# Kernel tuning notes

Measured on AMD Instinct MI355X. Metric: run time of the kernel, lower is better.

## Reference

```python
import jax, jax.numpy as jnp
import numpy as np

NEG_SLOPE = 0.2


def gat_conv(x, src, dst, W, a_src, a_dst, b, heads, ch, n_nodes):
    # x: [N, F_in] -> h: [N, H, C]
    h = (x @ W).reshape(n_nodes, heads, ch)
    alpha_src = (h * a_src).sum(-1)  # [N, H]
    alpha_dst = (h * a_dst).sum(-1)  # [N, H]
    e = jax.nn.leaky_relu(alpha_src[src] + alpha_dst[dst], NEG_SLOPE)  # [E, H]
    # segment softmax over destination neighborhoods (every node has a self-loop)
    m = jax.ops.segment_max(e, dst, num_segments=n_nodes)
    e = jnp.exp(e - m[dst])
    s = jax.ops.segment_sum(e, dst, num_segments=n_nodes)
    alpha = e / s[dst]  # [E, H]
    out = jax.ops.segment_sum(h[src] * alpha[:, :, None], dst, num_segments=n_nodes)
    return out.reshape(n_nodes, heads * ch) + b


def setup_inputs() -> dict:
    key = jax.random.key(0)
    ks = jax.random.split(key, 12)
    N, E = 50000, 800000
    F_in, HID, H, OUT = 128, 64, 2, 64
    x = jax.random.normal(ks[0], (N, F_in), dtype=jnp.float32)
    edge_index = jax.random.randint(ks[1], (2, E), 0, N, dtype=jnp.int64)
    s1 = 1.0 / np.sqrt(F_in)
    s2 = 1.0 / np.sqrt(H * HID)
    return {
        "x": x,
        "edge_index": edge_index,
        "W1": jax.random.normal(ks[2], (F_in, H * HID), dtype=jnp.float32) * s1,
        "att_src1": jax.random.normal(ks[3], (H, HID), dtype=jnp.float32) * s1,
        "att_dst1": jax.random.normal(ks[4], (H, HID), dtype=jnp.float32) * s1,
        "b1": jnp.zeros((H * HID,), dtype=jnp.float32),
        "W2": jax.random.normal(ks[5], (H * HID, OUT), dtype=jnp.float32) * s2,
        "att_src2": jax.random.normal(ks[6], (1, OUT), dtype=jnp.float32) * s2,
        "att_dst2": jax.random.normal(ks[7], (1, OUT), dtype=jnp.float32) * s2,
        "b2": jnp.zeros((OUT,), dtype=jnp.float32),
    }


def reference(x, edge_index, W1, att_src1, att_dst1, b1, W2, att_src2, att_dst2, b2):
    N = x.shape[0]
    # PyG GATConv adds self-loops by default
    loops = jnp.arange(N, dtype=edge_index.dtype)
    src = jnp.concatenate([edge_index[0], loops])
    dst = jnp.concatenate([edge_index[1], loops])
    h = gat_conv(x, src, dst, W1, att_src1, att_dst1, b1, 2, 64, N)
    h = jax.nn.relu(h)
    out = gat_conv(h, src, dst, W2, att_src2, att_dst2, b2, 1, 64, N)
    return jax.nn.sigmoid(out)
```

## Files before the change

### kernel.cpp

```cpp
#include <hip/hip_runtime.h>
#include <math.h>

#define N_NODES 50000
#define N_EDGES 800000
#define NEG_SLOPE 0.2f
#define NB_BKT  ((N_NODES + 127) / 128)
#define BKT_CAP 3200
#define P1_CHUNK 4096
#define NB_P1   ((N_EDGES + P1_CHUNK - 1) / P1_CHUNK)
#define NB_G1   ((N_NODES + 127) / 128)
#define CELL_CAP 48

typedef short bf16x8 __attribute__((ext_vector_type(8)));
typedef float f32x4 __attribute__((ext_vector_type(4)));

static __device__ __forceinline__ float lrelu(float v) {
    return v > 0.0f ? v : NEG_SLOPE * v;
}

static __device__ __forceinline__ unsigned short f2bf(float f) {
    unsigned b = __float_as_uint(f);
    return (unsigned short)((b + 0x7fffu + ((b >> 16) & 1u)) >> 16);
}

static __device__ __forceinline__ float bflo(unsigned u) { return __uint_as_float(u << 16); }
static __device__ __forceinline__ float bfhi(unsigned u) { return __uint_as_float(u & 0xffff0000u); }

static __device__ __forceinline__ int swz(int row, int k) {
    return row * 128 + ((((k >> 3) ^ (row & 15)) << 3) | (k & 7));
}
static __device__ __forceinline__ int swz64(int row, int c) {
    return row * 64 + ((((c >> 3) ^ (row & 7)) << 3) | (c & 7));
}

__global__ __launch_bounds__(256) void scatterP1_kernel(const int* __restrict__ ei,
                                                        int* __restrict__ cellcnt,
                                                        unsigned* __restrict__ cells) {
    __shared__ int cnt[NB_BKT];
    int tid = threadIdx.x;
    int c = blockIdx.x;
    for (int i = tid; i < NB_BKT; i += 256) cnt[i] = 0;
    __syncthreads();
    int cbase = c * P1_CHUNK;
    for (int i = tid; i < P1_CHUNK; i += 256) {
        int e = cbase + i;
        if (e >= N_EDGES) break;
        int s = ei[e];
        int d = ei[N_EDGES + e];
        int bk = d >> 7;
        int pos = atomicAdd(&cnt[bk], 1);
        if (pos < CELL_CAP)
            cells[(size_t)(c * NB_BKT + bk) * CELL_CAP + pos] =
                ((unsigned)s << 7) | (unsigned)(d & 127);
    }
    __syncthreads();
    for (int i = tid; i < NB_BKT; i += 256) {
        int v = cnt[i];
        cellcnt[c * NB_BKT + i] = v < CELL_CAP ? v : CELL_CAP;
    }
}

__global__ __launch_bounds__(256, 4) void fusedB_kernel(const float* __restrict__ x,
                                                        const float* __restrict__ W,
                                                        const float* __restrict__ a_src,
                                                        const float* __restrict__ a_dst,
                                                        unsigned short* __restrict__ h1b,
                                                        float* __restrict__ as_out,
                                                        float* __restrict__ ad_out,
                                                        const int* __restrict__ cellcnt,
                                                        const unsigned* __restrict__ cells,
                                                        int* __restrict__ offsets,
                                                        int* __restrict__ deg,
                                                        int* __restrict__ csr_src) {
    __shared__ __align__(16) unsigned char smem[32768];
    int tid = threadIdx.x;

    if (blockIdx.x < NB_BKT) {
        int* cnt   = (int*)smem;
        int* scn   = (int*)(smem + 1024);
        int* sst   = (int*)(smem + 2048);
        int* cincl = (int*)(smem + 3072);
        int* fkeys = (int*)(smem + 4096);
        int* lsrc  = (int*)(smem + 4096 + 4 * BKT_CAP);
        int t = tid;
        int b = blockIdx.x;
        int pbase = b * BKT_CAP;
        int node0 = b << 7;
        int nloc = N_NODES - node0; if (nloc > 128) nloc = 128;

        cnt[t] = (t < nloc) ? 1 : 0;
        cincl[t] = (t < NB_P1) ? cellcnt[t * NB_BKT + b] : 0;
        __syncthreads();
#pragma unroll
        for (int off = 1; off < 256; off <<= 1) {
            int u = (t >= off) ? cincl[t - off] : 0;
            __syncthreads();
            cincl[t] += u;
            __syncthreads();
        }
        int cntE = cincl[255];
        for (int j = t; j < cntE; j += 256) {
            int lo = 0, hi = NB_P1 - 1;
            while (lo < hi) {
                int mid = (lo + hi) >> 1;
                if (cincl[mid] <= j) lo = mid + 1; else hi = mid;
            }
            int cb2 = lo ? cincl[lo - 1] : 0;
            int k = (int)cells[(size_t)(lo * NB_BKT + b) * CELL_CAP + (j - cb2)];
            fkeys[j] = k;
            atomicAdd(&cnt[k & 127], 1);
        }
        if (t < nloc) fkeys[cntE + t] = ((node0 + t) << 7) | t;
        int cntE2 = cntE + nloc;
        __syncthreads();
        int v = cnt[t];
        scn[t] = v;
        __syncthreads();
#pragma unroll
        for (int off = 1; off < 256; off <<= 1) {
            int u = (t >= off) ? scn[t - off] : 0;
            __syncthreads();
            scn[t] += u;
            __syncthreads();
        }
        int lstart = scn[t] - v;
        sst[t] = lstart;
        cnt[t] = lstart;
        if (t < nloc) {
            offsets[node0 + t] = pbase + lstart;
            deg[node0 + t] = v;
        }
        __syncthreads();
        for (int j = t; j < cntE2; j += 256) {
            int k = fkeys[j];
            int p = atomicAdd(&cnt[k & 127], 1);
            lsrc[p] = k;
        }
        __syncthreads();
        for (int j = t; j < cntE2; j += 256) {
            int w = lsrc[j];
            int dl = w & 127;
            int st = sst[dl];
            int en = scn[dl];
            int r = 0;
            for (int k = st; k < en; ++k) {
                int wk = lsrc[k];
                r += (wk < w) ? 1 : ((wk == w && k < j) ? 1 : 0);
            }
            csr_src[pbase + st + r] = (int)(((unsigned)w) >> 7);
        }
        return;
    }

    unsigned short* wt = (unsigned short*)smem;
    int r0 = (blockIdx.x - NB_BKT) * 128;

    {
        int n = tid & 127;
        int c0 = (tid >> 7) * 8;
        for (int c = c0; c < c0 + 8; ++c) {
            int kb = c * 8;
            ushort4 lo, hi;
            lo.x = f2bf(W[(kb + 0) * 128 + n]);
            lo.y = f2bf(W[(kb + 1) * 128 + n]);
            lo.z = f2bf(W[(kb + 2) * 128 + n]);
            lo.w = f2bf(W[(kb + 3) * 128 + n]);
            hi.x = f2bf(W[(kb + 4) * 128 + n]);
            hi.y = f2bf(W[(kb + 5) * 128 + n]);
            hi.z = f2bf(W[(kb + 6) * 128 + n]);
            hi.w = f2bf(W[(kb + 7) * 128 + n]);
            int a = swz(n, kb);
            *(ushort4*)&wt[a] = lo;
            *(ushort4*)&wt[a + 4] = hi;
        }
    }
    __syncthreads();

    int wv = tid >> 6, lane = tid & 63, lm = lane & 15, quad = lane >> 4;
    int row0 = r0 + wv * 32 + lm;
    int row1 = row0 + 16;
    if (row0 > N_NODES - 1) row0 = N_NODES - 1;
    if (row1 > N_NODES - 1) row1 = N_NODES - 1;

    f32x4 acc[2][8];
#pragma unroll
    for (int m = 0; m < 2; ++m)
#pragma unroll
        for (int n = 0; n < 8; ++n) acc[m][n] = (f32x4){0.f, 0.f, 0.f, 0.f};

#pragma unroll
    for (int kc = 0; kc < 4; ++kc) {
        int kb = kc * 32 + quad * 8;
        float4 va0 = *(const float4*)&x[row0 * 128 + kb];
        float4 va1 = *(const float4*)&x[row0 * 128 + kb + 4];
        float4 vb0 = *(const float4*)&x[row1 * 128 + kb];
        float4 vb1 = *(const float4*)&x[row1 * 128 + kb + 4];
        bf16x8 a0, a1;
        a0[0] = (short)f2bf(va0.x); a0[1] = (short)f2bf(va0.y);
        a0[2] = (short)f2bf(va0.z); a0[3] = (short)f2bf(va0.w);
        a0[4] = (short)f2bf(va1.x); a0[5] = (short)f2bf(va1.y);
        a0[6] = (short)f2bf(va1.z); a0[7] = (short)f2bf(va1.w);
        a1[0] = (short)f2bf(vb0.x); a1[1] = (short)f2bf(vb0.y);
        a1[2] = (short)f2bf(vb0.z); a1[3] = (short)f2bf(vb0.w);
        a1[4] = (short)f2bf(vb1.x); a1[5] = (short)f2bf(vb1.y);
        a1[6] = (short)f2bf(vb1.z); a1[7] = (short)f2bf(vb1.w);
#pragma unroll
        for (int nt = 0; nt < 8; ++nt) {
            bf16x8 bfr = *(bf16x8*)&wt[swz(nt * 16 + lm, kb)];
            acc[0][nt] = __builtin_amdgcn_mfma_f32_16x16x32_bf16(a0, bfr, acc[0][nt], 0, 0, 0);
            acc[1][nt] = __builtin_amdgcn_mfma_f32_16x16x32_bf16(a1, bfr, acc[1][nt], 0, 0, 0);
        }
    }

    float asv[8], adv[8];
#pragma unroll
    for (int nt = 0; nt < 8; ++nt) {
        asv[nt] = a_src[nt * 16 + lm];
        adv[nt] = a_dst[nt * 16 + lm];
    }
#pragma unroll
    for (int mt = 0; mt < 2; ++mt) {
#pragma unroll
        for (int r = 0; r < 4; ++r) {
            float s0 = 0.f, s1 = 0.f, d0 = 0.f, d1 = 0.f;
#pragma unroll
            for (int nt = 0; nt < 4; ++nt) {
                s0 += acc[mt][nt][r] * asv[nt];
                d0 += acc[mt][nt][r] * adv[nt];
            }
#pragma unroll
            for (int nt = 4; nt < 8; ++nt) {
                s1 += acc[mt][nt][r] * asv[nt];
                d1 += acc[mt][nt][r] * adv[nt];
            }
#pragma unroll
            for (int m = 1; m < 16; m <<= 1) {
                s0 += __shfl_xor(s0, m, 64);
                s1 += __shfl_xor(s1, m, 64);
                d0 += __shfl_xor(d0, m, 64);
                d1 += __shfl_xor(d1, m, 64);
            }
            if (lm == 0) {
                int gr = r0 + wv * 32 + mt * 16 + quad * 4 + r;
                if (gr < N_NODES) {
                    as_out[gr * 2 + 0] = s0;
                    as_out[gr * 2 + 1] = s1;
                    ad_out[gr * 2 + 0] = d0;
                    ad_out[gr * 2 + 1] = d1;
                }
            }
        }
    }

    __syncthreads();
#pragma unroll
    for (int mt = 0; mt < 2; ++mt) {
#pragma unroll
        for (int nt = 0; nt < 8; ++nt) {
#pragma unroll
            for (int r = 0; r < 4; ++r) {
                int lrow = wv * 32 + mt * 16 + quad * 4 + r;
                wt[swz(lrow, nt * 16 + lm)] = f2bf(acc[mt][nt][r]);
            }
        }
    }
    __syncthreads();
    {
        int lrow = tid >> 1;
        int cb = (tid & 1) * 64;
        int gr = r0 + lrow;
        if (gr < N_NODES) {
            unsigned short* dst = h1b + (size_t)gr * 128 + cb;
#pragma unroll
            for (int c = 0; c < 8; ++c)
                *(uint4*)(dst + c * 8) = *(uint4*)&wt[swz(lrow, cb + c * 8)];
        }
    }
}

__global__ __launch_bounds__(256, 4) void gemm2_kernel(const unsigned short* __restrict__ xb,
                                                       const float* __restrict__ W,
                                                       const float* __restrict__ a_src,
                                                       const float* __restrict__ a_dst,
                                                       unsigned short* __restrict__ h2b,
                                                       float* __restrict__ as_out,
                                                       float* __restrict__ ad_out) {
    __shared__ unsigned short wt[64 * 128];
    int tid = threadIdx.x;
    int r0 = blockIdx.x * 128;

    {
        int n = tid & 63;
        int c0 = (tid >> 6) * 4;
        for (int c = c0; c < c0 + 4; ++c) {
            int kb = c * 8;
            ushort4 lo, hi;
            lo.x = f2bf(W[(kb + 0) * 64 + n]);
            lo.y = f2bf(W[(kb + 1) * 64 + n]);
            lo.z = f2bf(W[(kb + 2) * 64 + n]);
            lo.w = f2bf(W[(kb + 3) * 64 + n]);
            hi.x = f2bf(W[(kb + 4) * 64 + n]);
            hi.y = f2bf(W[(kb + 5) * 64 + n]);
            hi.z = f2bf(W[(kb + 6) * 64 + n]);
            hi.w = f2bf(W[(kb + 7) * 64 + n]);
            int a = swz(n, kb);
            *(ushort4*)&wt[a] = lo;
            *(ushort4*)&wt[a + 4] = hi;
        }
    }
    __syncthreads();

    int wv = tid >> 6, lane = tid & 63, lm = lane & 15, quad = lane >> 4;
    int row0 = r0 + wv * 32 + lm;
    int row1 = row0 + 16;
    if (row0 > N_NODES - 1) row0 = N_NODES - 1;
    if (row1 > N_NODES - 1) row1 = N_NODES - 1;

    f32x4 acc[2][4];
#pragma unroll
    for (int m = 0; m < 2; ++m)
#pragma unroll
        for (int n = 0; n < 4; ++n) acc[m][n] = (f32x4){0.f, 0.f, 0.f, 0.f};

#pragma unroll
    for (int kc = 0; kc < 4; ++kc) {
        int kb = kc * 32 + quad * 8;
        bf16x8 a0 = *(const bf16x8*)&xb[row0 * 128 + kb];
        bf16x8 a1 = *(const bf16x8*)&xb[row1 * 128 + kb];
#pragma unroll
        for (int nt = 0; nt < 4; ++nt) {
            bf16x8 b = *(bf16x8*)&wt[swz(nt * 16 + lm, kb)];
            acc[0][nt] = __builtin_amdgcn_mfma_f32_16x16x32_bf16(a0, b, acc[0][nt], 0, 0, 0);
            acc[1][nt] = __builtin_amdgcn_mfma_f32_16x16x32_bf16(a1, b, acc[1][nt], 0, 0, 0);
        }
    }

    float asv[4], adv[4];
#pragma unroll
    for (int nt = 0; nt < 4; ++nt) {
        asv[nt] = a_src[nt * 16 + lm];
        adv[nt] = a_dst[nt * 16 + lm];
    }
#pragma unroll
    for (int mt = 0; mt < 2; ++mt) {
#pragma unroll
        for (int r = 0; r < 4; ++r) {
            float s0 = 0.f, d0 = 0.f;
#pragma unroll
            for (int nt = 0; nt < 4; ++nt) {
                s0 += acc[mt][nt][r] * asv[nt];
                d0 += acc[mt][nt][r] * adv[nt];
            }
#pragma unroll
            for (int m = 1; m < 16; m <<= 1) {
                s0 += __shfl_xor(s0, m, 64);
                d0 += __shfl_xor(d0, m, 64);
            }
            if (lm == 0) {
                int gr = r0 + wv * 32 + mt * 16 + quad * 4 + r;
                if (gr < N_NODES) {
                    as_out[gr] = s0;
                    ad_out[gr] = d0;
                }
            }
        }
    }

    __syncthreads();
#pragma unroll
    for (int mt = 0; mt < 2; ++mt) {
#pragma unroll
        for (int nt = 0; nt < 4; ++nt) {
#pragma unroll
            for (int r = 0; r < 4; ++r) {
                int lrow = wv * 32 + mt * 16 + quad * 4 + r;
                wt[swz64(lrow, nt * 16 + lm)] = f2bf(acc[mt][nt][r]);
            }
        }
    }
    __syncthreads();
    {
        int lrow = tid >> 1;
        int cb = (tid & 1) * 32;
        int gr = r0 + lrow;
        if (gr < N_NODES) {
            unsigned short* dst = h2b + (size_t)gr * 64 + cb;
#pragma unroll
            for (int c = 0; c < 4; ++c)
                *(uint4*)(dst + c * 8) = *(uint4*)&wt[swz64(lrow, cb + c * 8)];
        }
    }
}

__global__ void agg1_kernel(const unsigned short* __restrict__ h1b,
                            const float* __restrict__ as1,
                            const float* __restrict__ ad1, const float* __restrict__ b1,
                            const int* __restrict__ offsets, const int* __restrict__ deg,
                            const int* __restrict__ csr_src,
                            unsigned short* __restrict__ out1b) {
    int wid = (blockIdx.x * blockDim.x + threadIdx.x) >> 6;
    if (wid >= N_NODES) return;
    int lane = threadIdx.x & 63;
    int cl = lane & 31;
    int half = lane >> 5;
    bool head1 = (cl >= 16);
    float da0 = ad1[wid * 2 + 0], da1 = ad1[wid * 2 + 1];
    int jb = offsets[wid], je = jb + deg[wid];
    float a0 = 0.f, a1 = 0.f, a2 = 0.f, a3 = 0.f;
    float psum0 = 0.f, psum1 = 0.f;

    for (int chunk = jb; chunk < je; chunk += 64) {
        int j = chunk + lane;
        int s = 0; float w0 = 0.f, w1 = 0.f;
        if (j < je) {
            s = csr_src[j];
            float2 av = *(const float2*)&as1[s * 2];
            w0 = __expf(lrelu(av.x + da0));
            w1 = __expf(lrelu(av.y + da1));
        }
        psum0 += w0; psum1 += w1;
        int cnt = je - chunk; if (cnt > 64) cnt = 64;
        for (int k = 0; k < cnt; k += 8) {
            int k0 = k + half, k1 = k + 2 + half, k2 = k + 4 + half, k3 = k + 6 + half;
            int ss0 = __shfl(s, k0, 64);
            int ss1 = __shfl(s, k1, 64);
            int ss2 = __shfl(s, k2, 64);
            int ss3 = __shfl(s, k3, 64);
            uint2 u0 = ((const uint2*)(h1b + (size_t)ss0 * 128))[cl];
            uint2 u1 = ((const uint2*)(h1b + (size_t)ss1 * 128))[cl];
            uint2 u2 = ((const uint2*)(h1b + (size_t)ss2 * 128))[cl];
            uint2 u3 = ((const uint2*)(h1b + (size_t)ss3 * 128))[cl];
            float p0 = __shfl(w0, k0, 64), q0 = __shfl(w1, k0, 64);
            float p1 = __shfl(w0, k1, 64), q1 = __shfl(w1, k1, 64);
            float p2 = __shfl(w0, k2, 64), q2 = __shfl(w1, k2, 64);
            float p3 = __shfl(w0, k3, 64), q3 = __shfl(w1, k3, 64);
            float bw0 = head1 ? q0 : p0;
            float bw1 = head1 ? q1 : p1;
            float bw2 = head1 ? q2 : p2;
            float bw3 = head1 ? q3 : p3;
            a0 += bw0 * bflo(u0.x); a1 += bw0 * bfhi(u0.x); a2 += bw0 * bflo(u0.y); a3 += bw0 * bfhi(u0.y);
            a0 += bw1 * bflo(u1.x); a1 += bw1 * bfhi(u1.x); a2 += bw1 * bflo(u1.y); a3 += bw1 * bfhi(u1.y);
            a0 += bw2 * bflo(u2.x); a1 += bw2 * bfhi(u2.x); a2 += bw2 * bflo(u2.y); a3 += bw2 * bfhi(u2.y);
            a0 += bw3 * bflo(u3.x); a1 += bw3 * bfhi(u3.x); a2 += bw3 * bflo(u3.y); a3 += bw3 * bfhi(u3.y);
        }
    }
#pragma unroll
    for (int m = 1; m < 64; m <<= 1) {
        psum0 += __shfl_xor(psum0, m, 64);
        psum1 += __shfl_xor(psum1, m, 64);
    }
    float o0 = __shfl(a0, cl + 32, 64);
    float o1 = __shfl(a1, cl + 32, 64);
    float o2 = __shfl(a2, cl + 32, 64);
    float o3 = __shfl(a3, cl + 32, 64);
    if (lane < 32) {
        float inv = 1.f / (head1 ? psum1 : psum0);
        float4 bv = *(const float4*)&b1[cl * 4];
        float v0 = (a0 + o0) * inv + bv.x;
        float v1 = (a1 + o1) * inv + bv.y;
        float v2 = (a2 + o2) * inv + bv.z;
        float v3 = (a3 + o3) * inv + bv.w;
        v0 = v0 > 0.f ? v0 : 0.f;
        v1 = v1 > 0.f ? v1 : 0.f;
        v2 = v2 > 0.f ? v2 : 0.f;
        v3 = v3 > 0.f ? v3 : 0.f;
        ushort4 p;
        p.x = f2bf(v0); p.y = f2bf(v1); p.z = f2bf(v2); p.w = f2bf(v3);
        *(ushort4*)&out1b[(size_t)wid * 128 + cl * 4] = p;
    }
}

__global__ void agg2_kernel(const unsigned short* __restrict__ h2b,
                            const float* __restrict__ as2,
                            const float* __restrict__ ad2, const float* __restrict__ b2,
                            const int* __restrict__ offsets, const int* __restrict__ deg,
                            const int* __restrict__ csr_src,
                            float* __restrict__ out) {
    int wid = (blockIdx.x * blockDim.x + threadIdx.x) >> 6;
    if (wid >= N_NODES) return;
    int lane = threadIdx.x & 63;
    int cl = lane & 31;
    int half = lane >> 5;
    float da = ad2[wid];
    int jb = offsets[wid], je = jb + deg[wid];
    float acc0 = 0.f, acc1 = 0.f, psum = 0.f;

    for (int chunk = jb; chunk < je; chunk += 64) {
        int j = chunk + lane;
        int s = 0; float w = 0.f;
        if (j < je) {
            s = csr_src[j];
            w = __expf(lrelu(as2[s] + da));
        }
        psum += w;
        int cnt = je - chunk; if (cnt > 64) cnt = 64;
        for (int k = 0; k < cnt; k += 8) {
            int k0 = k + half, k1 = k + 2 + half, k2 = k + 4 + half, k3 = k + 6 + half;
            int ss0 = __shfl(s, k0, 64);
            int ss1 = __shfl(s, k1, 64);
            int ss2 = __shfl(s, k2, 64);
            int ss3 = __shfl(s, k3, 64);
            unsigned u0 = ((const unsigned*)(h2b + (size_t)ss0 * 64))[cl];
            unsigned u1 = ((const unsigned*)(h2b + (size_t)ss1 * 64))[cl];
            unsigned u2 = ((const unsigned*)(h2b + (size_t)ss2 * 64))[cl];
            unsigned u3 = ((const unsigned*)(h2b + (size_t)ss3 * 64))[cl];
            float bw0 = __shfl(w, k0, 64);
            float bw1 = __shfl(w, k1, 64);
            float bw2 = __shfl(w, k2, 64);
            float bw3 = __shfl(w, k3, 64);
            acc0 += bw0 * bflo(u0); acc1 += bw0 * bfhi(u0);
            acc0 += bw1 * bflo(u1); acc1 += bw1 * bfhi(u1);
            acc0 += bw2 * bflo(u2); acc1 += bw2 * bfhi(u2);
            acc0 += bw3 * bflo(u3); acc1 += bw3 * bfhi(u3);
        }
    }
#pragma unroll
    for (int m = 1; m < 64; m <<= 1) psum += __shfl_xor(psum, m, 64);
    float o0 = __shfl(acc0, cl + 32, 64);
    float o1 = __shfl(acc1, cl + 32, 64);
    if (lane < 32) {
        float inv = 1.f / psum;
        float2 bv = *(const float2*)&b2[cl * 2];
        float v0 = (acc0 + o0) * inv + bv.x;
        float v1 = (acc1 + o1) * inv + bv.y;
        v0 = 1.f / (1.f + __expf(-v0));
        v1 = 1.f / (1.f + __expf(-v1));
        *(float2*)&out[(size_t)wid * 64 + cl * 2] = make_float2(v0, v1);
    }
}

extern "C" void kernel_launch(void* const* d_in, const int* in_sizes, int n_in,
                              void* d_out, int out_size, void* d_ws, size_t ws_size,
                              hipStream_t stream) {
    const float* x     = (const float*)d_in[0];
    const int*   ei    = (const int*)d_in[1];
    const float* W1    = (const float*)d_in[2];
    const float* asrc1 = (const float*)d_in[3];
    const float* adst1 = (const float*)d_in[4];
    const float* b1    = (const float*)d_in[5];
    const float* W2    = (const float*)d_in[6];
    const float* asrc2 = (const float*)d_in[7];
    const float* adst2 = (const float*)d_in[8];
    const float* b2    = (const float*)d_in[9];
    float* out = (float*)d_out;

    float* ws = (float*)d_ws;
    size_t off = 0;
    float* as1  = ws + off; off += (size_t)N_NODES * 2;
    float* ad1  = ws + off; off += (size_t)N_NODES * 2;
    float* as2  = ws + off; off += (size_t)N_NODES;
    float* ad2  = ws + off; off += (size_t)N_NODES;
    unsigned short* h1b   = (unsigned short*)(ws + off); off += (size_t)N_NODES * 64;
    unsigned short* out1b = (unsigned short*)(ws + off); off += (size_t)N_NODES * 64;
    unsigned short* h2b   = (unsigned short*)(ws + off); off += (size_t)N_NODES * 32;
    int* offsets = (int*)(ws + off);
    int* deg     = offsets + N_NODES;
    int* csr_src = deg + N_NODES;
    int* cellcnt = csr_src + NB_BKT * BKT_CAP;
    unsigned* cells = (unsigned*)(cellcnt + NB_P1 * NB_BKT);

    scatterP1_kernel<<<NB_P1, 256, 0, stream>>>(ei, cellcnt, cells);
    fusedB_kernel<<<NB_BKT + NB_G1, 256, 0, stream>>>(x, W1, asrc1, adst1, h1b, as1, ad1,
                                                      cellcnt, cells, offsets, deg, csr_src);
    agg1_kernel<<<(N_NODES * 64 + 255) / 256, 256, 0, stream>>>(h1b, as1, ad1, b1, offsets, deg, csr_src, out1b);
    gemm2_kernel<<<NB_G1, 256, 0, stream>>>(out1b, W2, asrc2, adst2, h2b, as2, ad2);
    agg2_kernel<<<(N_NODES * 64 + 255) / 256, 256, 0, stream>>>(h2b, as2, ad2, b2, offsets, deg, csr_src, out);
}
```

Before: 193.4 us.

## Process two destination nodes per wavefront in GAT aggregation kernels

Each wavefront in agg1 and agg2 now handles two destination nodes, i and i+N/2, and the grid is halved to match. The first chunk of csr_src indices and attention weights for both nodes is prefetched up front, so those latency-bound loads overlap. Accumulation moves to float2 vector types, which may let the compiler emit packed FMAs, and launch bounds are added. The cost is more registers per lane, the two nodes' gather loops still run one after the other, and half as many waves are available to hide memory latency.

Result: faster. 189.2 us, median of 2 (-2.2%).

```diff
diff --git a/kernel.cpp b/kernel.cpp
--- a/kernel.cpp
+++ b/kernel.cpp
@@ -2,6 +2,7 @@
 #include <math.h>
 
 #define N_NODES 50000
+#define NH (N_NODES / 2)
 #define N_EDGES 800000
 #define NEG_SLOPE 0.2f
 #define NB_BKT  ((N_NODES + 127) / 128)
@@ -13,6 +14,7 @@
 
 typedef short bf16x8 __attribute__((ext_vector_type(8)));
 typedef float f32x4 __attribute__((ext_vector_type(4)));
+typedef float f32x2 __attribute__((ext_vector_type(2)));
 
 static __device__ __forceinline__ float lrelu(float v) {
     return v > 0.0f ? v : NEG_SLOPE * v;
@@ -25,6 +27,9 @@
 
 static __device__ __forceinline__ float bflo(unsigned u) { return __uint_as_float(u << 16); }
 static __device__ __forceinline__ float bfhi(unsigned u) { return __uint_as_float(u & 0xffff0000u); }
+static __device__ __forceinline__ f32x2 bfp(unsigned u) {
+    f32x2 r; r[0] = bflo(u); r[1] = bfhi(u); return r;
+}
 
 static __device__ __forceinline__ int swz(int row, int k) {
     return row * 128 + ((((k >> 3) ^ (row & 15)) << 3) | (k & 7));
@@ -392,34 +397,59 @@
     }
 }
 
-__global__ void agg1_kernel(const unsigned short* __restrict__ h1b,
+__global__ __launch_bounds__(256) void agg1_kernel(const unsigned short* __restrict__ h1b,
                             const float* __restrict__ as1,
                             const float* __restrict__ ad1, const float* __restrict__ b1,
                             const int* __restrict__ offsets, const int* __restrict__ deg,
                             const int* __restrict__ csr_src,
                             unsigned short* __restrict__ out1b) {
-    int wid = (blockIdx.x * blockDim.x + threadIdx.x) >> 6;
-    if (wid >= N_NODES) return;
+    int wv = (blockIdx.x * blockDim.x + threadIdx.x) >> 6;
+    if (wv >= NH) return;
     int lane = threadIdx.x & 63;
     int cl = lane & 31;
     int half = lane >> 5;
     bool head1 = (cl >= 16);
-    float da0 = ad1[wid * 2 + 0], da1 = ad1[wid * 2 + 1];
-    int jb = offsets[wid], je = jb + deg[wid];
-    float a0 = 0.f, a1 = 0.f, a2 = 0.f, a3 = 0.f;
-    float psum0 = 0.f, psum1 = 0.f;
-
-    for (int chunk = jb; chunk < je; chunk += 64) {
-        int j = chunk + lane;
-        int s = 0; float w0 = 0.f, w1 = 0.f;
-        if (j < je) {
-            s = csr_src[j];
-            float2 av = *(const float2*)&as1[s * 2];
-            w0 = __expf(lrelu(av.x + da0));
-            w1 = __expf(lrelu(av.y + da1));
-        }
-        psum0 += w0; psum1 += w1;
-        int cnt = je - chunk; if (cnt > 64) cnt = 64;
+    int widA = wv, widB = wv + NH;
+
+    float2 daA = *(const float2*)&ad1[widA * 2];
+    float2 daB = *(const float2*)&ad1[widB * 2];
+    int jbA = offsets[widA], jeA = jbA + deg[widA];
+    int jbB = offsets[widB], jeB = jbB + deg[widB];
+
+    int jA = jbA + lane, jB = jbB + lane;
+    int spA = 0, spB = 0;
+    float wpA0 = 0.f, wpA1 = 0.f, wpB0 = 0.f, wpB1 = 0.f;
+    if (jA < jeA) spA = csr_src[jA];
+    if (jB < jeB) spB = csr_src[jB];
+    if (jA < jeA) {
+        float2 av = *(const float2*)&as1[spA * 2];
+        wpA0 = __expf(lrelu(av.x + daA.x));
+        wpA1 = __expf(lrelu(av.y + daA.y));
+    }
+    if (jB < jeB) {
+        float2 av = *(const float2*)&as1[spB * 2];
+        wpB0 = __expf(lrelu(av.x + daB.x));
+        wpB1 = __expf(lrelu(av.y + daB.y));
+    }
+
+    f32x2 A0A = (f32x2){0.f, 0.f}, A1A = (f32x2){0.f, 0.f};
+    f32x2 A0B = (f32x2){0.f, 0.f}, A1B = (f32x2){0.f, 0.f};
+    float psA0 = 0.f, psA1 = 0.f, psB0 = 0.f, psB1 = 0.f;
+
+    for (int chunk = jbA; chunk < jeA; chunk += 64) {
+        int s; float w0, w1;
+        if (chunk == jbA) { s = spA; w0 = wpA0; w1 = wpA1; }
+        else {
+            int j = chunk + lane; s = 0; w0 = 0.f; w1 = 0.f;
+            if (j < jeA) {
+                s = csr_src[j];
+                float2 av = *(const float2*)&as1[s * 2];
+                w0 = __expf(lrelu(av.x + daA.x));
+                w1 = __expf(lrelu(av.y + daA.y));
+            }
+        }
+        psA0 += w0; psA1 += w1;
+        int cnt = jeA - chunk; if (cnt > 64) cnt = 64;
         for (int k = 0; k < cnt; k += 8) {
             int k0 = k + half, k1 = k + 2 + half, k2 = k + 4 + half, k3 = k + 6 + half;
             int ss0 = __shfl(s, k0, 64);
@@ -438,62 +468,139 @@
             float bw1 = head1 ? q1 : p1;
             float bw2 = head1 ? q2 : p2;
             float bw3 = head1 ? q3 : p3;
-            a0 += bw0 * bflo(u0.x); a1 += bw0 * bfhi(u0.x); a2 += bw0 * bflo(u0.y); a3 += bw0 * bfhi(u0.y);
-            a0 += bw1 * bflo(u1.x); a1 += bw1 * bfhi(u1.x); a2 += bw1 * bflo(u1.y); a3 += bw1 * bfhi(u1.y);
-            a0 += bw2 * bflo(u2.x); a1 += bw2 * bfhi(u2.x); a2 += bw2 * bflo(u2.y); a3 += bw2 * bfhi(u2.y);
-            a0 += bw3 * bflo(u3.x); a1 += bw3 * bfhi(u3.x); a2 += bw3 * bflo(u3.y); a3 += bw3 * bfhi(u3.y);
-        }
-    }
+            A0A += (f32x2){bw0, bw0} * bfp(u0.x); A1A += (f32x2){bw0, bw0} * bfp(u0.y);
+            A0A += (f32x2){bw1, bw1} * bfp(u1.x); A1A += (f32x2){bw1, bw1} * bfp(u1.y);
+            A0A += (f32x2){bw2, bw2} * bfp(u2.x); A1A += (f32x2){bw2, bw2} * bfp(u2.y);
+            A0A += (f32x2){bw3, bw3} * bfp(u3.x); A1A += (f32x2){bw3, bw3} * bfp(u3.y);
+        }
+    }
+
+    for (int chunk = jbB; chunk < jeB; chunk += 64) {
+        int s; float w0, w1;
+        if (chunk == jbB) { s = spB; w0 = wpB0; w1 = wpB1; }
+        else {
+            int j = chunk + lane; s = 0; w0 = 0.f; w1 = 0.f;
+            if (j < jeB) {
+                s = csr_src[j];
+                float2 av = *(const float2*)&as1[s * 2];
+                w0 = __expf(lrelu(av.x + daB.x));
+                w1 = __expf(lrelu(av.y + daB.y));
+            }
+        }
+        psB0 += w0; psB1 += w1;
+        int cnt = jeB - chunk; if (cnt > 64) cnt = 64;
+        for (int k = 0; k < cnt; k += 8) {
+            int k0 = k + half, k1 = k + 2 + half, k2 = k + 4 + half, k3 = k + 6 + half;
+            int ss0 = __shfl(s, k0, 64);
+            int ss1 = __shfl(s, k1, 64);
+            int ss2 = __shfl(s, k2, 64);
+            int ss3 = __shfl(s, k3, 64);
+            uint2 u0 = ((const uint2*)(h1b + (size_t)ss0 * 128))[cl];
+            uint2 u1 = ((const uint2*)(h1b + (size_t)ss1 * 128))[cl];
+            uint2 u2 = ((const uint2*)(h1b + (size_t)ss2 * 128))[cl];
+            uint2 u3 = ((const uint2*)(h1b + (size_t)ss3 * 128))[cl];
+            float p0 = __shfl(w0, k0, 64), q0 = __shfl(w1, k0, 64);
+            float p1 = __shfl(w0, k1, 64), q1 = __shfl(w1, k1, 64);
+            float p2 = __shfl(w0, k2, 64), q2 = __shfl(w1, k2, 64);
+            float p3 = __shfl(w0, k3, 64), q3 = __shfl(w1, k3, 64);
+            float bw0 = head1 ? q0 : p0;
+            float bw1 = head1 ? q1 : p1;
+            float bw2 = head1 ? q2 : p2;
+            float bw3 = head1 ? q3 : p3;
+            A0B += (f32x2){bw0, bw0} * bfp(u0.x); A1B += (f32x2){bw0, bw0} * bfp(u0.y);
+            A0B += (f32x2){bw1, bw1} * bfp(u1.x); A1B += (f32x2){bw1, bw1} * bfp(u1.y);
+            A0B += (f32x2){bw2, bw2} * bfp(u2.x); A1B += (f32x2){bw2, bw2} * bfp(u2.y);
+            A0B += (f32x2){bw3, bw3} * bfp(u3.x); A1B += (f32x2){bw3, bw3} * bfp(u3.y);
+        }
+    }
+
 #pragma unroll
     for (int m = 1; m < 64; m <<= 1) {
-        psum0 += __shfl_xor(psum0, m, 64);
-        psum1 += __shfl_xor(psum1, m, 64);
-    }
-    float o0 = __shfl(a0, cl + 32, 64);
-    float o1 = __shfl(a1, cl + 32, 64);
-    float o2 = __shfl(a2, cl + 32, 64);
-    float o3 = __shfl(a3, cl + 32, 64);
+        psA0 += __shfl_xor(psA0, m, 64);
+        psA1 += __shfl_xor(psA1, m, 64);
+        psB0 += __shfl_xor(psB0, m, 64);
+        psB1 += __shfl_xor(psB1, m, 64);
+    }
+    float aA0 = A0A[0], aA1 = A0A[1], aA2 = A1A[0], aA3 = A1A[1];
+    float aB0 = A0B[0], aB1 = A0B[1], aB2 = A1B[0], aB3 = A1B[1];
+    float oA0 = __shfl(aA0, cl + 32, 64);
+    float oA1 = __shfl(aA1, cl + 32, 64);
+    float oA2 = __shfl(aA2, cl + 32, 64);
+    float oA3 = __shfl(aA3, cl + 32, 64);
+    float oB0 = __shfl(aB0, cl + 32, 64);
+    float oB1 = __shfl(aB1, cl + 32, 64);
+    float oB2 = __shfl(aB2, cl + 32, 64);
+    float oB3 = __shfl(aB3, cl + 32, 64);
     if (lane < 32) {
-        float inv = 1.f / (head1 ? psum1 : psum0);
         float4 bv = *(const float4*)&b1[cl * 4];
-        float v0 = (a0 + o0) * inv + bv.x;
-        float v1 = (a1 + o1) * inv + bv.y;
-        float v2 = (a2 + o2) * inv + bv.z;
-        float v3 = (a3 + o3) * inv + bv.w;
-        v0 = v0 > 0.f ? v0 : 0.f;
-        v1 = v1 > 0.f ? v1 : 0.f;
-        v2 = v2 > 0.f ? v2 : 0.f;
-        v3 = v3 > 0.f ? v3 : 0.f;
-        ushort4 p;
-        p.x = f2bf(v0); p.y = f2bf(v1); p.z = f2bf(v2); p.w = f2bf(v3);
-        *(ushort4*)&out1b[(size_t)wid * 128 + cl * 4] = p;
-    }
-}
-
-__global__ void agg2_kernel(const unsigned short* __restrict__ h2b,
+        {
+            float inv = 1.f / (head1 ? psA1 : psA0);
+            float v0 = (aA0 + oA0) * inv + bv.x;
+            float v1 = (aA1 + oA1) * inv + bv.y;
+            float v2 = (aA2 + oA2) * inv + bv.z;
+            float v3 = (aA3 + oA3) * inv + bv.w;
+            v0 = v0 > 0.f ? v0 : 0.f;
+            v1 = v1 > 0.f ? v1 : 0.f;
+            v2 = v2 > 0.f ? v2 : 0.f;
+            v3 = v3 > 0.f ? v3 : 0.f;
+            ushort4 p;
+            p.x = f2bf(v0); p.y = f2bf(v1); p.z = f2bf(v2); p.w = f2bf(v3);
+            *(ushort4*)&out1b[(size_t)widA * 128 + cl * 4] = p;
+        }
+        {
+            float inv = 1.f / (head1 ? psB1 : psB0);
+            float v0 = (aB0 + oB0) * inv + bv.x;
+            float v1 = (aB1 + oB1) * inv + bv.y;
+            float v2 = (aB2 + oB2) * inv + bv.z;
+            float v3 = (aB3 + oB3) * inv + bv.w;
+            v0 = v0 > 0.f ? v0 : 0.f;
+            v1 = v1 > 0.f ? v1 : 0.f;
+            v2 = v2 > 0.f ? v2 : 0.f;
+            v3 = v3 > 0.f ? v3 : 0.f;
+            ushort4 p;
+            p.x = f2bf(v0); p.y = f2bf(v1); p.z = f2bf(v2); p.w = f2bf(v3);
+            *(ushort4*)&out1b[(size_t)widB * 128 + cl * 4] = p;
+        }
+    }
+}
+
+__global__ __launch_bounds__(256) void agg2_kernel(const unsigned short* __restrict__ h2b,
                             const float* __restrict__ as2,
                             const float* __restrict__ ad2, const float* __restrict__ b2,
                             const int* __restrict__ offsets, const int* __restrict__ deg,
                             const int* __restrict__ csr_src,
                             float* __restrict__ out) {
-    int wid = (blockIdx.x * blockDim.x + threadIdx.x) >> 6;
-    if (wid >= N_NODES) return;
+    int wv = (blockIdx.x * blockDim.x + threadIdx.x) >> 6;
+    if (wv >= NH) return;
     int lane = threadIdx.x & 63;
     int cl = lane & 31;
     int half = lane >> 5;
-    float da = ad2[wid];
-    int jb = offsets[wid], je = jb + deg[wid];
-    float acc0 = 0.f, acc1 = 0.f, psum = 0.f;
-
-    for (int chunk = jb; chunk < je; chunk += 64) {
-        int j = chunk + lane;
-        int s = 0; float w = 0.f;
-        if (j < je) {
-            s = csr_src[j];
-            w = __expf(lrelu(as2[s] + da));
-        }
-        psum += w;
-        int cnt = je - chunk; if (cnt > 64) cnt = 64;
+    int widA = wv, widB = wv + NH;
+
+    float daA = ad2[widA], daB = ad2[widB];
+    int jbA = offsets[widA], jeA = jbA + deg[widA];
+    int jbB = offsets[widB], jeB = jbB + deg[widB];
+
+    int jA = jbA + lane, jB = jbB + lane;
+    int spA = 0, spB = 0;
+    float wpA = 0.f, wpB = 0.f;
+    if (jA < jeA) spA = csr_src[jA];
+    if (jB < jeB) spB = csr_src[jB];
+    if (jA < jeA) wpA = __expf(lrelu(as2[spA] + daA));
+    if (jB < jeB) wpB = __expf(lrelu(as2[spB] + daB));
+
+    f32x2 AA = (f32x2){0.f, 0.f}, AB = (f32x2){0.f, 0.f};
+    float psA = 0.f, psB = 0.f;
+
+    for (int chunk = jbA; chunk < jeA; chunk += 64) {
+        int s; float w;
+        if (chunk == jbA) { s = spA; w = wpA; }
+        else {
+            int j = chunk + lane; s = 0; w = 0.f;
+            if (j < jeA) { s = csr_src[j]; w = __expf(lrelu(as2[s] + daA)); }
+        }
+        psA += w;
+        int cnt = jeA - chunk; if (cnt > 64) cnt = 64;
         for (int k = 0; k < cnt; k += 8) {
             int k0 = k + half, k1 = k + 2 + half, k2 = k + 4 + half, k3 = k + 6 + half;
             int ss0 = __shfl(s, k0, 64);
@@ -508,24 +615,71 @@
             float bw1 = __shfl(w, k1, 64);
             float bw2 = __shfl(w, k2, 64);
             float bw3 = __shfl(w, k3, 64);
-            acc0 += bw0 * bflo(u0); acc1 += bw0 * bfhi(u0);
-            acc0 += bw1 * bflo(u1); acc1 += bw1 * bfhi(u1);
-            acc0 += bw2 * bflo(u2); acc1 += bw2 * bfhi(u2);
-            acc0 += bw3 * bflo(u3); acc1 += bw3 * bfhi(u3);
-        }
-    }
-#pragma unroll
-    for (int m = 1; m < 64; m <<= 1) psum += __shfl_xor(psum, m, 64);
-    float o0 = __shfl(acc0, cl + 32, 64);
-    float o1 = __shfl(acc1, cl + 32, 64);
+            AA += (f32x2){bw0, bw0} * bfp(u0);
+            AA += (f32x2){bw1, bw1} * bfp(u1);
+            AA += (f32x2){bw2, bw2} * bfp(u2);
+            AA += (f32x2){bw3, bw3} * bfp(u3);
+        }
+    }
+
+    for (int chunk = jbB; chunk < jeB; chunk += 64) {
+        int s; float w;
+        if (chunk == jbB) { s = spB; w = wpB; }
+        else {
+            int j = chunk + lane; s = 0; w = 0.f;
+            if (j < jeB) { s = csr_src[j]; w = __expf(lrelu(as2[s] + daB)); }
+        }
+        psB += w;
+        int cnt = jeB - chunk; if (cnt > 64) cnt = 64;
+        for (int k = 0; k < cnt; k += 8) {
+            int k0 = k + half, k1 = k + 2 + half, k2 = k + 4 + half, k3 = k + 6 + half;
+            int ss0 = __shfl(s, k0, 64);
+            int ss1 = __shfl(s, k1, 64);
+            int ss2 = __shfl(s, k2, 64);
+            int ss3 = __shfl(s, k3, 64);
+            unsigned u0 = ((const unsigned*)(h2b + (size_t)ss0 * 64))[cl];
+            unsigned u1 = ((const unsigned*)(h2b + (size_t)ss1 * 64))[cl];
+            unsigned u2 = ((const unsigned*)(h2b + (size_t)ss2 * 64))[cl];
+            unsigned u3 = ((const unsigned*)(h2b + (size_t)ss3 * 64))[cl];
+            float bw0 = __shfl(w, k0, 64);
+            float bw1 = __shfl(w, k1, 64);
+            float bw2 = __shfl(w, k2, 64);
+            float bw3 = __shfl(w, k3, 64);
+            AB += (f32x2){bw0, bw0} * bfp(u0);
+            AB += (f32x2){bw1, bw1} * bfp(u1);
+            AB += (f32x2){bw2, bw2} * bfp(u2);
+            AB += (f32x2){bw3, bw3} * bfp(u3);
+        }
+    }
+
+#pragma unroll
+    for (int m = 1; m < 64; m <<= 1) {
+        psA += __shfl_xor(psA, m, 64);
+        psB += __shfl_xor(psB, m, 64);
+    }
+    float aA0 = AA[0], aA1 = AA[1], aB0 = AB[0], aB1 = AB[1];
+    float oA0 = __shfl(aA0, cl + 32, 64);
+    float oA1 = __shfl(aA1, cl + 32, 64);
+    float oB0 = __shfl(aB0, cl + 32, 64);
+    float oB1 = __shfl(aB1, cl + 32, 64);
     if (lane < 32) {
-        float inv = 1.f / psum;
         float2 bv = *(const float2*)&b2[cl * 2];
-        float v0 = (acc0 + o0) * inv + bv.x;
-        float v1 = (acc1 + o1) * inv + bv.y;
-        v0 = 1.f / (1.f + __expf(-v0));
-        v1 = 1.f / (1.f + __expf(-v1));
-        *(float2*)&out[(size_t)wid * 64 + cl * 2] = make_float2(v0, v1);
+        {
+            float inv = 1.f / psA;
+            float v0 = (aA0 + oA0) * inv + bv.x;
+            float v1 = (aA1 + oA1) * inv + bv.y;
+            v0 = 1.f / (1.f + __expf(-v0));
+            v1 = 1.f / (1.f + __expf(-v1));
+            *(float2*)&out[(size_t)widA * 64 + cl * 2] = make_float2(v0, v1);
+        }
+        {
+            float inv = 1.f / psB;
+            float v0 = (aB0 + oB0) * inv + bv.x;
+            float v1 = (aB1 + oB1) * inv + bv.y;
+            v0 = 1.f / (1.f + __expf(-v0));
+            v1 = 1.f / (1.f + __expf(-v1));
+            *(float2*)&out[(size_t)widB * 64 + cl * 2] = make_float2(v0, v1);
+        }
     }
 }
 
@@ -562,7 +716,7 @@
     scatterP1_kernel<<<NB_P1, 256, 0, stream>>>(ei, cellcnt, cells);
     fusedB_kernel<<<NB_BKT + NB_G1, 256, 0, stream>>>(x, W1, asrc1, adst1, h1b, as1, ad1,
                                                       cellcnt, cells, offsets, deg, csr_src);
-    agg1_kernel<<<(N_NODES * 64 + 255) / 256, 256, 0, stream>>>(h1b, as1, ad1, b1, offsets, deg, csr_src, out1b);
+    agg1_kernel<<<(NH * 64 + 255) / 256, 256, 0, stream>>>(h1b, as1, ad1, b1, offsets, deg, csr_src, out1b);
     gemm2_kernel<<<NB_G1, 256, 0, stream>>>(out1b, W2, asrc2, adst2, h2b, as2, ad2);
-    agg2_kernel<<<(N_NODES * 64 + 255) / 256, 256, 0, stream>>>(h2b, as2, ad2, b2, offsets, deg, csr_src, out);
-}
+    agg2_kernel<<<(NH * 64 + 255) / 256, 256, 0, stream>>>(h2b, as2, ad2, b2, offsets, deg, csr_src, out);
+}
```

## Process four destination nodes per wavefront in aggregation kernels

Applied to the files above, without the earlier changes.

Each wavefront in agg1 and agg2 now handles four destination nodes, strided by N/4, instead of one. The offsets, degree, first-chunk source indices and attention weights for all four nodes are loaded up front so their memory latencies overlap. Accumulation uses packed float2 vectors, which may let the compiler emit packed FMA instructions. In exchange the grid has four times fewer wavefronts and each thread holds more registers, and the nodes are still processed one after another inside a wave, so latency hiding may depend on occupancy.

Measured after the change: 198.9 us. 1.03x slower.

```diff
diff --git a/kernel.cpp b/kernel.cpp
--- a/kernel.cpp
+++ b/kernel.cpp
@@ -2,6 +2,7 @@
 #include <math.h>
 
 #define N_NODES 50000
+#define NQ (N_NODES / 4)
 #define N_EDGES 800000
 #define NEG_SLOPE 0.2f
 #define NB_BKT  ((N_NODES + 127) / 128)
@@ -13,6 +14,7 @@
 
 typedef short bf16x8 __attribute__((ext_vector_type(8)));
 typedef float f32x4 __attribute__((ext_vector_type(4)));
+typedef float f32x2 __attribute__((ext_vector_type(2)));
 
 static __device__ __forceinline__ float lrelu(float v) {
     return v > 0.0f ? v : NEG_SLOPE * v;
@@ -25,6 +27,9 @@
 
 static __device__ __forceinline__ float bflo(unsigned u) { return __uint_as_float(u << 16); }
 static __device__ __forceinline__ float bfhi(unsigned u) { return __uint_as_float(u & 0xffff0000u); }
+static __device__ __forceinline__ f32x2 bfp(unsigned u) {
+    f32x2 r; r[0] = bflo(u); r[1] = bfhi(u); return r;
+}
 
 static __device__ __forceinline__ int swz(int row, int k) {
     return row * 128 + ((((k >> 3) ^ (row & 15)) << 3) | (k & 7));
@@ -392,140 +397,219 @@
     }
 }
 
-__global__ void agg1_kernel(const unsigned short* __restrict__ h1b,
+__global__ __launch_bounds__(256) void agg1_kernel(const unsigned short* __restrict__ h1b,
                             const float* __restrict__ as1,
                             const float* __restrict__ ad1, const float* __restrict__ b1,
                             const int* __restrict__ offsets, const int* __restrict__ deg,
                             const int* __restrict__ csr_src,
                             unsigned short* __restrict__ out1b) {
-    int wid = (blockIdx.x * blockDim.x + threadIdx.x) >> 6;
-    if (wid >= N_NODES) return;
+    int wv = (blockIdx.x * blockDim.x + threadIdx.x) >> 6;
+    if (wv >= NQ) return;
     int lane = threadIdx.x & 63;
     int cl = lane & 31;
     int half = lane >> 5;
     bool head1 = (cl >= 16);
-    float da0 = ad1[wid * 2 + 0], da1 = ad1[wid * 2 + 1];
-    int jb = offsets[wid], je = jb + deg[wid];
-    float a0 = 0.f, a1 = 0.f, a2 = 0.f, a3 = 0.f;
-    float psum0 = 0.f, psum1 = 0.f;
-
-    for (int chunk = jb; chunk < je; chunk += 64) {
-        int j = chunk + lane;
-        int s = 0; float w0 = 0.f, w1 = 0.f;
-        if (j < je) {
-            s = csr_src[j];
-            float2 av = *(const float2*)&as1[s * 2];
-            w0 = __expf(lrelu(av.x + da0));
-            w1 = __expf(lrelu(av.y + da1));
-        }
-        psum0 += w0; psum1 += w1;
-        int cnt = je - chunk; if (cnt > 64) cnt = 64;
-        for (int k = 0; k < cnt; k += 8) {
-            int k0 = k + half, k1 = k + 2 + half, k2 = k + 4 + half, k3 = k + 6 + half;
-            int ss0 = __shfl(s, k0, 64);
-            int ss1 = __shfl(s, k1, 64);
-            int ss2 = __shfl(s, k2, 64);
-            int ss3 = __shfl(s, k3, 64);
-            uint2 u0 = ((const uint2*)(h1b + (size_t)ss0 * 128))[cl];
-            uint2 u1 = ((const uint2*)(h1b + (size_t)ss1 * 128))[cl];
-            uint2 u2 = ((const uint2*)(h1b + (size_t)ss2 * 128))[cl];
-            uint2 u3 = ((const uint2*)(h1b + (size_t)ss3 * 128))[cl];
-            float p0 = __shfl(w0, k0, 64), q0 = __shfl(w1, k0, 64);
-            float p1 = __shfl(w0, k1, 64), q1 = __shfl(w1, k1, 64);
-            float p2 = __shfl(w0, k2, 64), q2 = __shfl(w1, k2, 64);
-            float p3 = __shfl(w0, k3, 64), q3 = __shfl(w1, k3, 64);
-            float bw0 = head1 ? q0 : p0;
-            float bw1 = head1 ? q1 : p1;
-            float bw2 = head1 ? q2 : p2;
-            float bw3 = head1 ? q3 : p3;
-            a0 += bw0 * bflo(u0.x); a1 += bw0 * bfhi(u0.x); a2 += bw0 * bflo(u0.y); a3 += bw0 * bfhi(u0.y);
-            a0 += bw1 * bflo(u1.x); a1 += bw1 * bfhi(u1.x); a2 += bw1 * bflo(u1.y); a3 += bw1 * bfhi(u1.y);
-            a0 += bw2 * bflo(u2.x); a1 += bw2 * bfhi(u2.x); a2 += bw2 * bflo(u2.y); a3 += bw2 * bfhi(u2.y);
-            a0 += bw3 * bflo(u3.x); a1 += bw3 * bfhi(u3.x); a2 += bw3 * bflo(u3.y); a3 += bw3 * bfhi(u3.y);
-        }
-    }
+
+    int jb[4], je[4], sp[4];
+    float2 da[4];
+    float wp0[4], wp1[4];
+#pragma unroll
+    for (int i = 0; i < 4; ++i) {
+        int wid = wv + i * NQ;
+        da[i] = *(const float2*)&ad1[wid * 2];
+        jb[i] = offsets[wid];
+        je[i] = jb[i] + deg[wid];
+    }
+#pragma unroll
+    for (int i = 0; i < 4; ++i) {
+        int j = jb[i] + lane;
+        sp[i] = (j < je[i]) ? csr_src[j] : 0;
+    }
+#pragma unroll
+    for (int i = 0; i < 4; ++i) {
+        int j = jb[i] + lane;
+        wp0[i] = 0.f; wp1[i] = 0.f;
+        if (j < je[i]) {
+            float2 av = *(const float2*)&as1[sp[i] * 2];
+            wp0[i] = __expf(lrelu(av.x + da[i].x));
+            wp1[i] = __expf(lrelu(av.y + da[i].y));
+        }
+    }
+
+    f32x2 A0[4], A1[4];
+    float ps0[4], ps1[4];
+#pragma unroll
+    for (int i = 0; i < 4; ++i) {
+        A0[i] = (f32x2){0.f, 0.f}; A1[i] = (f32x2){0.f, 0.f};
+        ps0[i] = 0.f; ps1[i] = 0.f;
+    }
+
+#pragma unroll
+    for (int i = 0; i < 4; ++i) {
+        for (int chunk = jb[i]; chunk < je[i]; chunk += 64) {
+            int s; float w0, w1;
+            if (chunk == jb[i]) { s = sp[i]; w0 = wp0[i]; w1 = wp1[i]; }
+            else {
+                int j = chunk + lane; s = 0; w0 = 0.f; w1 = 0.f;
+                if (j < je[i]) {
+                    s = csr_src[j];
+                    float2 av = *(const float2*)&as1[s * 2];
+                    w0 = __expf(lrelu(av.x + da[i].x));
+                    w1 = __expf(lrelu(av.y + da[i].y));
+                }
+            }
+            ps0[i] += w0; ps1[i] += w1;
+            int cnt = je[i] - chunk; if (cnt > 64) cnt = 64;
+            for (int k = 0; k < cnt; k += 8) {
+                int k0 = k + half, k1 = k + 2 + half, k2 = k + 4 + half, k3 = k + 6 + half;
+                int ss0 = __shfl(s, k0, 64);
+                int ss1 = __shfl(s, k1, 64);
+                int ss2 = __shfl(s, k2, 64);
+                int ss3 = __shfl(s, k3, 64);
+                uint2 u0 = ((const uint2*)(h1b + (size_t)ss0 * 128))[cl];
+                uint2 u1 = ((const uint2*)(h1b + (size_t)ss1 * 128))[cl];
+                uint2 u2 = ((const uint2*)(h1b + (size_t)ss2 * 128))[cl];
+                uint2 u3 = ((const uint2*)(h1b + (size_t)ss3 * 128))[cl];
+                float p0 = __shfl(w0, k0, 64), q0 = __shfl(w1, k0, 64);
+                float p1 = __shfl(w0, k1, 64), q1 = __shfl(w1, k1, 64);
+                float p2 = __shfl(w0, k2, 64), q2 = __shfl(w1, k2, 64);
+                float p3 = __shfl(w0, k3, 64), q3 = __shfl(w1, k3, 64);
+                float bw0 = head1 ? q0 : p0;
+                float bw1 = head1 ? q1 : p1;
+                float bw2 = head1 ? q2 : p2;
+                float bw3 = head1 ? q3 : p3;
+                A0[i] += (f32x2){bw0, bw0} * bfp(u0.x); A1[i] += (f32x2){bw0, bw0} * bfp(u0.y);
+                A0[i] += (f32x2){bw1, bw1} * bfp(u1.x); A1[i] += (f32x2){bw1, bw1} * bfp(u1.y);
+                A0[i] += (f32x2){bw2, bw2} * bfp(u2.x); A1[i] += (f32x2){bw2, bw2} * bfp(u2.y);
+                A0[i] += (f32x2){bw3, bw3} * bfp(u3.x); A1[i] += (f32x2){bw3, bw3} * bfp(u3.y);
+            }
+        }
+    }
+
 #pragma unroll
     for (int m = 1; m < 64; m <<= 1) {
-        psum0 += __shfl_xor(psum0, m, 64);
-        psum1 += __shfl_xor(psum1, m, 64);
-    }
-    float o0 = __shfl(a0, cl + 32, 64);
-    float o1 = __shfl(a1, cl + 32, 64);
-    float o2 = __shfl(a2, cl + 32, 64);
-    float o3 = __shfl(a3, cl + 32, 64);
-    if (lane < 32) {
-        float inv = 1.f / (head1 ? psum1 : psum0);
-        float4 bv = *(const float4*)&b1[cl * 4];
-        float v0 = (a0 + o0) * inv + bv.x;
-        float v1 = (a1 + o1) * inv + bv.y;
-        float v2 = (a2 + o2) * inv + bv.z;
-        float v3 = (a3 + o3) * inv + bv.w;
-        v0 = v0 > 0.f ? v0 : 0.f;
-        v1 = v1 > 0.f ? v1 : 0.f;
-        v2 = v2 > 0.f ? v2 : 0.f;
-        v3 = v3 > 0.f ? v3 : 0.f;
-        ushort4 p;
-        p.x = f2bf(v0); p.y = f2bf(v1); p.z = f2bf(v2); p.w = f2bf(v3);
-        *(ushort4*)&out1b[(size_t)wid * 128 + cl * 4] = p;
-    }
-}
-
-__global__ void agg2_kernel(const unsigned short* __restrict__ h2b,
+#pragma unroll
+        for (int i = 0; i < 4; ++i) {
+            ps0[i] += __shfl_xor(ps0[i], m, 64);
+            ps1[i] += __shfl_xor(ps1[i], m, 64);
+        }
+    }
+    float4 bv;
+    if (lane < 32) bv = *(const float4*)&b1[cl * 4];
+#pragma unroll
+    for (int i = 0; i < 4; ++i) {
+        float a0 = A0[i][0], a1 = A0[i][1], a2 = A1[i][0], a3 = A1[i][1];
+        float o0 = __shfl(a0, cl + 32, 64);
+        float o1 = __shfl(a1, cl + 32, 64);
+        float o2 = __shfl(a2, cl + 32, 64);
+        float o3 = __shfl(a3, cl + 32, 64);
+        if (lane < 32) {
+            float inv = 1.f / (head1 ? ps1[i] : ps0[i]);
+            float v0 = (a0 + o0) * inv + bv.x;
+            float v1 = (a1 + o1) * inv + bv.y;
+            float v2 = (a2 + o2) * inv + bv.z;
+            float v3 = (a3 + o3) * inv + bv.w;
+            v0 = v0 > 0.f ? v0 : 0.f;
+            v1 = v1 > 0.f ? v1 : 0.f;
+            v2 = v2 > 0.f ? v2 : 0.f;
+            v3 = v3 > 0.f ? v3 : 0.f;
+            ushort4 p;
+            p.x = f2bf(v0); p.y = f2bf(v1); p.z = f2bf(v2); p.w = f2bf(v3);
+            *(ushort4*)&out1b[(size_t)(wv + i * NQ) * 128 + cl * 4] = p;
+        }
+    }
+}
+
+__global__ __launch_bounds__(256) void agg2_kernel(const unsigned short* __restrict__ h2b,
                             const float* __restrict__ as2,
                             const float* __restrict__ ad2, const float* __restrict__ b2,
                             const int* __restrict__ offsets, const int* __restrict__ deg,
                             const int* __restrict__ csr_src,
                             float* __restrict__ out) {
-    int wid = (blockIdx.x * blockDim.x + threadIdx.x) >> 6;
-    if (wid >= N_NODES) return;
+    int wv = (blockIdx.x * blockDim.x + threadIdx.x) >> 6;
+    if (wv >= NQ) return;
     int lane = threadIdx.x & 63;
     int cl = lane & 31;
     int half = lane >> 5;
-    float da = ad2[wid];
-    int jb = offsets[wid], je = jb + deg[wid];
-    float acc0 = 0.f, acc1 = 0.f, psum = 0.f;
-
-    for (int chunk = jb; chunk < je; chunk += 64) {
-        int j = chunk + lane;
-        int s = 0; float w = 0.f;
-        if (j < je) {
-            s = csr_src[j];
-            w = __expf(lrelu(as2[s] + da));
-        }
-        psum += w;
-        int cnt = je - chunk; if (cnt > 64) cnt = 64;
-        for (int k = 0; k < cnt; k += 8) {
-            int k0 = k + half, k1 = k + 2 + half, k2 = k + 4 + half, k3 = k + 6 + half;
-            int ss0 = __shfl(s, k0, 64);
-            int ss1 = __shfl(s, k1, 64);
-            int ss2 = __shfl(s, k2, 64);
-            int ss3 = __shfl(s, k3, 64);
-            unsigned u0 = ((const unsigned*)(h2b + (size_t)ss0 * 64))[cl];
-            unsigned u1 = ((const unsigned*)(h2b + (size_t)ss1 * 64))[cl];
-            unsigned u2 = ((const unsigned*)(h2b + (size_t)ss2 * 64))[cl];
-            unsigned u3 = ((const unsigned*)(h2b + (size_t)ss3 * 64))[cl];
-            float bw0 = __shfl(w, k0, 64);
-            float bw1 = __shfl(w, k1, 64);
-            float bw2 = __shfl(w, k2, 64);
-            float bw3 = __shfl(w, k3, 64);
-            acc0 += bw0 * bflo(u0); acc1 += bw0 * bfhi(u0);
-            acc0 += bw1 * bflo(u1); acc1 += bw1 * bfhi(u1);
-            acc0 += bw2 * bflo(u2); acc1 += bw2 * bfhi(u2);
-            acc0 += bw3 * bflo(u3); acc1 += bw3 * bfhi(u3);
-        }
-    }
-#pragma unroll
-    for (int m = 1; m < 64; m <<= 1) psum += __shfl_xor(psum, m, 64);
-    float o0 = __shfl(acc0, cl + 32, 64);
-    float o1 = __shfl(acc1, cl + 32, 64);
-    if (lane < 32) {
-        float inv = 1.f / psum;
-        float2 bv = *(const float2*)&b2[cl * 2];
-        float v0 = (acc0 + o0) * inv + bv.x;
-        float v1 = (acc1 + o1) * inv + bv.y;
-        v0 = 1.f / (1.f + __expf(-v0));
-        v1 = 1.f / (1.f + __expf(-v1));
-        *(float2*)&out[(size_t)wid * 64 + cl * 2] = make_float2(v0, v1);
+
+    int jb[4], je[4], sp[4];
+    float da[4], wp[4];
+#pragma unroll
+    for (int i = 0; i < 4; ++i) {
+        int wid = wv + i * NQ;
+        da[i] = ad2[wid];
+        jb[i] = offsets[wid];
+        je[i] = jb[i] + deg[wid];
+    }
+#pragma unroll
+    for (int i = 0; i < 4; ++i) {
+        int j = jb[i] + lane;
+        sp[i] = (j < je[i]) ? csr_src[j] : 0;
+    }
+#pragma unroll
+    for (int i = 0; i < 4; ++i) {
+        int j = jb[i] + lane;
+        wp[i] = (j < je[i]) ? __expf(lrelu(as2[sp[i]] + da[i])) : 0.f;
+    }
+
+    f32x2 A[4];
+    float ps[4];
+#pragma unroll
+    for (int i = 0; i < 4; ++i) { A[i] = (f32x2){0.f, 0.f}; ps[i] = 0.f; }
+
+#pragma unroll
+    for (int i = 0; i < 4; ++i) {
+        for (int chunk = jb[i]; chunk < je[i]; chunk += 64) {
+            int s; float w;
+            if (chunk == jb[i]) { s = sp[i]; w = wp[i]; }
+            else {
+                int j = chunk + lane; s = 0; w = 0.f;
+                if (j < je[i]) { s = csr_src[j]; w = __expf(lrelu(as2[s] + da[i])); }
+            }
+            ps[i] += w;
+            int cnt = je[i] - chunk; if (cnt > 64) cnt = 64;
+            for (int k = 0; k < cnt; k += 8) {
+                int k0 = k + half, k1 = k + 2 + half, k2 = k + 4 + half, k3 = k + 6 + half;
+                int ss0 = __shfl(s, k0, 64);
+                int ss1 = __shfl(s, k1, 64);
+                int ss2 = __shfl(s, k2, 64);
+                int ss3 = __shfl(s, k3, 64);
+                unsigned u0 = ((const unsigned*)(h2b + (size_t)ss0 * 64))[cl];
+                unsigned u1 = ((const unsigned*)(h2b + (size_t)ss1 * 64))[cl];
+                unsigned u2 = ((const unsigned*)(h2b + (size_t)ss2 * 64))[cl];
+                unsigned u3 = ((const unsigned*)(h2b + (size_t)ss3 * 64))[cl];
+                float bw0 = __shfl(w, k0, 64);
+                float bw1 = __shfl(w, k1, 64);
+                float bw2 = __shfl(w, k2, 64);
+                float bw3 = __shfl(w, k3, 64);
+                A[i] += (f32x2){bw0, bw0} * bfp(u0);
+                A[i] += (f32x2){bw1, bw1} * bfp(u1);
+                A[i] += (f32x2){bw2, bw2} * bfp(u2);
+                A[i] += (f32x2){bw3, bw3} * bfp(u3);
+            }
+        }
+    }
+
+#pragma unroll
+    for (int m = 1; m < 64; m <<= 1) {
+#pragma unroll
+        for (int i = 0; i < 4; ++i) ps[i] += __shfl_xor(ps[i], m, 64);
+    }
+    float2 bv;
+    if (lane < 32) bv = *(const float2*)&b2[cl * 2];
+#pragma unroll
+    for (int i = 0; i < 4; ++i) {
+        float a0 = A[i][0], a1 = A[i][1];
+        float o0 = __shfl(a0, cl + 32, 64);
+        float o1 = __shfl(a1, cl + 32, 64);
+        if (lane < 32) {
+            float inv = 1.f / ps[i];
+            float v0 = (a0 + o0) * inv + bv.x;
+            float v1 = (a1 + o1) * inv + bv.y;
+            v0 = 1.f / (1.f + __expf(-v0));
+            v1 = 1.f / (1.f + __expf(-v1));
+            *(float2*)&out[(size_t)(wv + i * NQ) * 64 + cl * 2] = make_float2(v0, v1);
+        }
     }
 }
 
@@ -562,7 +646,7 @@
     scatterP1_kernel<<<NB_P1, 256, 0, stream>>>(ei, cellcnt, cells);
     fusedB_kernel<<<NB_BKT + NB_G1, 256, 0, stream>>>(x, W1, asrc1, adst1, h1b, as1, ad1,
                                                       cellcnt, cells, offsets, deg, csr_src);
-    agg1_kernel<<<(N_NODES * 64 + 255) / 256, 256, 0, stream>>>(h1b, as1, ad1, b1, offsets, deg, csr_src, out1b);
+    agg1_kernel<<<(NQ * 64 + 255) / 256, 256, 0, stream>>>(h1b, as1, ad1, b1, offsets, deg, csr_src, out1b);
     gemm2_kernel<<<NB_G1, 256, 0, stream>>>(out1b, W2, asrc2, adst2, h2b, as2, ad2);
-    agg2_kernel<<<(N_NODES * 64 + 255) / 256, 256, 0, stream>>>(h2b, as2, ad2, b2, offsets, deg, csr_src, out);
-}
+    agg2_kernel<<<(NQ * 64 + 255) / 256, 256, 0, stream>>>(h2b, as2, ad2, b2, offsets, deg, csr_src, out);
+}
```
